# Kernel tuning notes

Measured on AMD Instinct MI355X. Metric: run time of the kernel, lower is better.

Reference implementation:

```python
import jax, jax.numpy as jnp
import numpy as np

N_NODES = 50000
N_EDGES = 1000000
D_IN = 64
D_OUT = 64
EDGE_DIM = 16
NEG_SLOPE = 0.2


def setup_inputs() -> dict:
    key = jax.random.key(0)
    ks = jax.random.split(key, 10)
    x = jax.random.normal(ks[0], (N_NODES, D_IN), dtype=jnp.float32)
    edge_index = jax.random.randint(ks[1], (2, N_EDGES), 0, N_NODES, dtype=jnp.int64)
    edge_attr = jax.random.normal(ks[2], (N_EDGES, EDGE_DIM), dtype=jnp.float32)
    s = 0.1
    W_l = jax.random.normal(ks[3], (D_IN, D_OUT), dtype=jnp.float32) * s
    b_l = jnp.zeros((D_OUT,), dtype=jnp.float32)
    W_r = jax.random.normal(ks[4], (D_IN, D_OUT), dtype=jnp.float32) * s
    b_r = jnp.zeros((D_OUT,), dtype=jnp.float32)
    W_e = jax.random.normal(ks[5], (EDGE_DIM, D_OUT), dtype=jnp.float32) * s
    att = jax.random.normal(ks[6], (D_OUT,), dtype=jnp.float32) * s
    bias = jnp.zeros((D_OUT,), dtype=jnp.float32)
    return {"x": x, "edge_index": edge_index, "edge_attr": edge_attr,
            "W_l": W_l, "b_l": b_l, "W_r": W_r, "b_r": b_r,
            "W_e": W_e, "att": att, "bias": bias}


def reference(x, edge_index, edge_attr, W_l, b_l, W_r, b_r, W_e, att, bias):
    # GATv2Conv (heads=1, concat) with edge features, share_weights=False.
    src = edge_index[0]  # message source j
    dst = edge_index[1]  # aggregation target i
    n = x.shape[0]

    x_l = x @ W_l + b_l          # [N, C] source transform
    x_r = x @ W_r + b_r          # [N, C] target transform
    e = edge_attr @ W_e          # [E, C] edge transform (no bias in lin_edge)

    # per-edge GATv2 attention logit: a^T LeakyReLU(x_l[j] + x_r[i] + e)
    h = jax.nn.leaky_relu(x_l[src] + x_r[dst] + e, NEG_SLOPE)  # [E, C]
    logits = h @ att  # [E]

    # segment softmax over incoming edges of each target node
    m = jax.ops.segment_max(logits, dst, num_segments=n)        # [N]
    ex = jnp.exp(logits - m[dst])                               # [E]
    denom = jax.ops.segment_sum(ex, dst, num_segments=n)       # [N]
    alpha = ex / (denom[dst] + 1e-16)                           # [E]

    # weighted scatter-add of source messages x_l[j]
    out = jax.ops.segment_sum(alpha[:, None] * x_l[src], dst, num_segments=n)
    return out + bias
```

## Files before the change

kernel.cpp:

```cpp
#include <hip/hip_runtime.h>
#include <hip/hip_bf16.h>
#include <math.h>

#define N_NODES 50000
#define N_EDGES 1000000
#define D 64
#define ED 16
#define NEG 0.2f

__device__ __forceinline__ float wave_sum(float v) {
  #pragma unroll
  for (int m = 32; m >= 1; m >>= 1) v += __shfl_xor(v, m, 64);
  return v;
}

__global__ void k_init(int* __restrict__ cursor) {
  int i = blockIdx.x * 256 + threadIdx.x;
  if (i < N_NODES) cursor[i] = 0;
}

__global__ __launch_bounds__(256) void k_transform(
    const float* __restrict__ x,
    const float* __restrict__ Wl, const float* __restrict__ bl,
    const float* __restrict__ Wr, const float* __restrict__ br,
    __hip_bfloat16* __restrict__ xlb, float* __restrict__ xr) {
  __shared__ float sW[2 * D * D];
  float* sWl = sW;
  float* sWr = sW + D * D;
  int t = threadIdx.x;
  for (int q = t; q < D * D / 4; q += 256) {
    ((float4*)sWl)[q] = ((const float4*)Wl)[q];
    ((float4*)sWr)[q] = ((const float4*)Wr)[q];
  }
  __syncthreads();
  int lane = t & 63;
  int row = blockIdx.x * 4 + (t >> 6);
  if (row >= N_NODES) return;
  float xv = x[row * D + lane];
  float accl = bl[lane], accr = br[lane];
  #pragma unroll
  for (int k = 0; k < D; k++) {
    float xk = __shfl(xv, k, 64);
    accl = fmaf(xk, sWl[k * D + lane], accl);
    accr = fmaf(xk, sWr[k * D + lane], accr);
  }
  xlb[row * D + lane] = __float2bfloat16(accl);
  xr[row * D + lane] = accr;
}

__global__ void k_hist(const int* __restrict__ ei, int* __restrict__ cursor) {
  int e = blockIdx.x * 256 + threadIdx.x;
  if (e < N_EDGES) atomicAdd(&cursor[ei[N_EDGES + e]], 1);
}

__global__ void k_scan_a(const int* __restrict__ counts, int* __restrict__ row_start,
                         int* __restrict__ bsum) {
  __shared__ int sb[256];
  int t = threadIdx.x;
  int i = blockIdx.x * 256 + t;
  int v = (i < N_NODES) ? counts[i] : 0;
  sb[t] = v;
  __syncthreads();
  for (int off = 1; off < 256; off <<= 1) {
    int add = (t >= off) ? sb[t - off] : 0;
    __syncthreads();
    sb[t] += add;
    __syncthreads();
  }
  if (i < N_NODES) row_start[i] = sb[t] - v;
  if (t == 255) bsum[blockIdx.x] = sb[t];
}
__global__ void k_scan_b(int* __restrict__ bsum, int nb) {
  __shared__ int sb[256];
  int t = threadIdx.x;
  int v = (t < nb) ? bsum[t] : 0;
  sb[t] = v;
  __syncthreads();
  for (int off = 1; off < 256; off <<= 1) {
    int add = (t >= off) ? sb[t - off] : 0;
    __syncthreads();
    sb[t] += add;
    __syncthreads();
  }
  if (t < nb) bsum[t] = sb[t] - v;
}
__global__ void k_scan_c(int* __restrict__ row_start, const int* __restrict__ bsum,
                         int* __restrict__ cursor) {
  int t = threadIdx.x;
  int i = blockIdx.x * 256 + t;
  if (i < N_NODES) {
    int r = row_start[i] + bsum[blockIdx.x];
    row_start[i] = r;
    cursor[i] = r;
  }
  if (i == 0) row_start[N_NODES] = N_EDGES;
}

__global__ void k_scatter(const int* __restrict__ ei, int* __restrict__ cursor,
                          int* __restrict__ eid_perm, int* __restrict__ src_perm) {
  int e = blockIdx.x * 256 + threadIdx.x;
  if (e >= N_EDGES) return;
  int s = ei[e];
  int d = ei[N_EDGES + e];
  int pos = atomicAdd(&cursor[d], 1);
  eid_perm[pos] = e;
  src_perm[pos] = s;
}

__global__ __launch_bounds__(256) void k_fused(
    const float* __restrict__ ea, const float* __restrict__ We,
    const float* __restrict__ att,
    const __hip_bfloat16* __restrict__ xlb, const float* __restrict__ xr,
    const int* __restrict__ row_start, const int* __restrict__ eid_perm,
    const int* __restrict__ src_perm, const float* __restrict__ bias,
    float* __restrict__ out) {
  __shared__ float sWe[ED * D];
  __shared__ float satt[D];
  int t = threadIdx.x;
  for (int q = t; q < ED * D / 4; q += 256) ((float4*)sWe)[q] = ((const float4*)We)[q];
  if (t < D) satt[t] = att[t];
  __syncthreads();
  int lane = t & 63;
  int n = blockIdx.x * 4 + (t >> 6);
  if (n >= N_NODES) return;
  int start = row_start[n];
  int end = row_start[n + 1];

  float xrv = xr[(size_t)n * D + lane];
  float av = satt[lane];
  float m = -INFINITY, lsum = 0.f, O = 0.f;

  for (int i = start; i < end; ++i) {
    int e = __builtin_amdgcn_readfirstlane(eid_perm[i]);
    int s = __builtin_amdgcn_readfirstlane(src_perm[i]);
    float xlv = __bfloat162float(xlb[(size_t)s * D + lane]);
    float eav = (lane < ED) ? ea[(size_t)e * ED + lane] : 0.f;
    float acc = 0.f;
    #pragma unroll
    for (int k = 0; k < ED; k++) {
      float ek = __shfl(eav, k, 64);
      acc = fmaf(ek, sWe[k * D + lane], acc);
    }
    float h = xlv + xrv + acc;
    h = (h > 0.f) ? h : NEG * h;
    float logit = wave_sum(h * av);
    float mn = fmaxf(m, logit);
    float sc = __expf(m - mn);
    float p = __expf(logit - mn);
    lsum = fmaf(lsum, sc, p);
    O = O * sc + p * xlv;
    m = mn;
  }
  out[(size_t)n * D + lane] = O / (lsum + 1e-16f) + bias[lane];
}

static inline char* align_up(char* p, size_t a) {
  return (char*)(((uintptr_t)p + a - 1) & ~(uintptr_t)(a - 1));
}

extern "C" void kernel_launch(void* const* d_in, const int* in_sizes, int n_in,
                              void* d_out, int out_size, void* d_ws, size_t ws_size,
                              hipStream_t stream) {
  const float* x   = (const float*)d_in[0];
  const int* ei    = (const int*)d_in[1];
  const float* ea  = (const float*)d_in[2];
  const float* Wl  = (const float*)d_in[3];
  const float* bl  = (const float*)d_in[4];
  const float* Wr  = (const float*)d_in[5];
  const float* br  = (const float*)d_in[6];
  const float* We  = (const float*)d_in[7];
  const float* att = (const float*)d_in[8];
  const float* bias = (const float*)d_in[9];
  float* out = (float*)d_out;

  char* w = (char*)d_ws;
  __hip_bfloat16* xlb = (__hip_bfloat16*)w; w = align_up(w + (size_t)N_NODES * D * 2, 256);
  float* xr       = (float*)w; w = align_up(w + (size_t)N_NODES * D * 4, 256);
  int* row_start  = (int*)w;   w = align_up(w + (size_t)(N_NODES + 1) * 4, 256);
  int* cursor     = (int*)w;   w = align_up(w + (size_t)N_NODES * 4, 256);
  int* bsum       = (int*)w;   w = align_up(w + 256 * 4, 256);
  int* eid_perm   = (int*)w;   w = align_up(w + (size_t)N_EDGES * 4, 256);
  int* src_perm   = (int*)w;   w = align_up(w + (size_t)N_EDGES * 4, 256);

  const int NB = (N_NODES + 255) / 256;

  k_init<<<NB, 256, 0, stream>>>(cursor);
  k_transform<<<N_NODES / 4, 256, 0, stream>>>(x, Wl, bl, Wr, br, xlb, xr);
  k_hist<<<(N_EDGES + 255) / 256, 256, 0, stream>>>(ei, cursor);
  k_scan_a<<<NB, 256, 0, stream>>>(cursor, row_start, bsum);
  k_scan_b<<<1, 256, 0, stream>>>(bsum, NB);
  k_scan_c<<<NB, 256, 0, stream>>>(row_start, bsum, cursor);
  k_scatter<<<(N_EDGES + 255) / 256, 256, 0, stream>>>(ei, cursor, eid_perm, src_perm);
  k_fused<<<(N_NODES + 3) / 4, 256, 0, stream>>>(ea, We, att, xlb, xr, row_start,
                                                 eid_perm, src_perm, bias, out);
}
```

Measured before the change: 536.5 us.

## Pack edge permutation into int2 and software-prefetch next edge's gathers

Merges the separate edge-id and source-id permutation arrays into one int2 array, so scatter does one 8-byte store and the fused kernel does one load per edge. The fused kernel's per-node loop is software-pipelined: the next edge's bf16 x_l row and edge_attr row are issued before the current edge's math, and the permutation entry two ahead is loaded as well. This targets the latency of the serial dependent gathers in the online-softmax loop, at the cost of extra registers and redundant clamped loads at the end of each segment.

```diff
diff --git a/kernel.cpp b/kernel.cpp
--- a/kernel.cpp
+++ b/kernel.cpp
@@ -97,23 +97,21 @@
 }
 
 __global__ void k_scatter(const int* __restrict__ ei, int* __restrict__ cursor,
-                          int* __restrict__ eid_perm, int* __restrict__ src_perm) {
+                          int2* __restrict__ perm) {
   int e = blockIdx.x * 256 + threadIdx.x;
   if (e >= N_EDGES) return;
   int s = ei[e];
   int d = ei[N_EDGES + e];
   int pos = atomicAdd(&cursor[d], 1);
-  eid_perm[pos] = e;
-  src_perm[pos] = s;
+  perm[pos] = make_int2(e, s);
 }
 
 __global__ __launch_bounds__(256) void k_fused(
     const float* __restrict__ ea, const float* __restrict__ We,
     const float* __restrict__ att,
     const __hip_bfloat16* __restrict__ xlb, const float* __restrict__ xr,
-    const int* __restrict__ row_start, const int* __restrict__ eid_perm,
-    const int* __restrict__ src_perm, const float* __restrict__ bias,
-    float* __restrict__ out) {
+    const int* __restrict__ row_start, const int2* __restrict__ perm,
+    const float* __restrict__ bias, float* __restrict__ out) {
   __shared__ float sWe[ED * D];
   __shared__ float satt[D];
   int t = threadIdx.x;
@@ -130,26 +128,44 @@
   float av = satt[lane];
   float m = -INFINITY, lsum = 0.f, O = 0.f;
 
-  for (int i = start; i < end; ++i) {
-    int e = __builtin_amdgcn_readfirstlane(eid_perm[i]);
-    int s = __builtin_amdgcn_readfirstlane(src_perm[i]);
-    float xlv = __bfloat162float(xlb[(size_t)s * D + lane]);
-    float eav = (lane < ED) ? ea[(size_t)e * ED + lane] : 0.f;
-    float acc = 0.f;
-    #pragma unroll
-    for (int k = 0; k < ED; k++) {
-      float ek = __shfl(eav, k, 64);
-      acc = fmaf(ek, sWe[k * D + lane], acc);
+  const unsigned short* xlr16 = (const unsigned short*)xlb;
+
+  if (start < end) {
+    int2 p0 = perm[start];
+    int e0 = __builtin_amdgcn_readfirstlane(p0.x);
+    int s0 = __builtin_amdgcn_readfirstlane(p0.y);
+    unsigned short xlr = xlr16[(size_t)s0 * D + lane];
+    float eav = (lane < ED) ? ea[(size_t)e0 * ED + lane] : 0.f;
+    int i1 = (start + 1 < end) ? start + 1 : start;
+    int2 pp = perm[i1];
+
+    for (int i = start; i < end; ++i) {
+      int e_n = __builtin_amdgcn_readfirstlane(pp.x);
+      int s_n = __builtin_amdgcn_readfirstlane(pp.y);
+      unsigned short xlr_n = xlr16[(size_t)s_n * D + lane];
+      float eav_n = (lane < ED) ? ea[(size_t)e_n * ED + lane] : 0.f;
+      int i2 = (i + 2 < end) ? i + 2 : i1;
+      pp = perm[i2];
+
+      float xlv = __uint_as_float(((unsigned)xlr) << 16);
+      float acc = 0.f;
+      #pragma unroll
+      for (int k = 0; k < ED; k++) {
+        float ek = __shfl(eav, k, 64);
+        acc = fmaf(ek, sWe[k * D + lane], acc);
+      }
+      float h = xlv + xrv + acc;
+      h = (h > 0.f) ? h : NEG * h;
+      float logit = wave_sum(h * av);
+      float mn = fmaxf(m, logit);
+      float sc = __expf(m - mn);
+      float p = __expf(logit - mn);
+      lsum = fmaf(lsum, sc, p);
+      O = O * sc + p * xlv;
+      m = mn;
+      xlr = xlr_n;
+      eav = eav_n;
     }
-    float h = xlv + xrv + acc;
-    h = (h > 0.f) ? h : NEG * h;
-    float logit = wave_sum(h * av);
-    float mn = fmaxf(m, logit);
-    float sc = __expf(m - mn);
-    float p = __expf(logit - mn);
-    lsum = fmaf(lsum, sc, p);
-    O = O * sc + p * xlv;
-    m = mn;
   }
   out[(size_t)n * D + lane] = O / (lsum + 1e-16f) + bias[lane];
 }
@@ -179,8 +195,7 @@
   int* row_start  = (int*)w;   w = align_up(w + (size_t)(N_NODES + 1) * 4, 256);
   int* cursor     = (int*)w;   w = align_up(w + (size_t)N_NODES * 4, 256);
   int* bsum       = (int*)w;   w = align_up(w + 256 * 4, 256);
-  int* eid_perm   = (int*)w;   w = align_up(w + (size_t)N_EDGES * 4, 256);
-  int* src_perm   = (int*)w;   w = align_up(w + (size_t)N_EDGES * 4, 256);
+  int2* perm      = (int2*)w;  w = align_up(w + (size_t)N_EDGES * 8, 256);
 
   const int NB = (N_NODES + 255) / 256;
 
@@ -190,7 +205,7 @@
   k_scan_a<<<NB, 256, 0, stream>>>(cursor, row_start, bsum);
   k_scan_b<<<1, 256, 0, stream>>>(bsum, NB);
   k_scan_c<<<NB, 256, 0, stream>>>(row_start, bsum, cursor);
-  k_scatter<<<(N_EDGES + 255) / 256, 256, 0, stream>>>(ei, cursor, eid_perm, src_perm);
+  k_scatter<<<(N_EDGES + 255) / 256, 256, 0, stream>>>(ei, cursor, perm);
   k_fused<<<(N_NODES + 3) / 4, 256, 0, stream>>>(ea, We, att, xlb, xr, row_start,
-                                                 eid_perm, src_perm, bias, out);
-}
+                                                 perm, bias, out);
+}
```

Result: no change. 537.4 us (+0.2%).
